# Performance work log

Measured on AMD Instinct MI355X. Metric: run time of the kernel, lower is better.

Reference implementation:

```python
import jax, jax.numpy as jnp
import numpy as np

B, CIN, H, W = 8, 128, 64, 64
COUT = 128
UP = 2
KH = KW = 2 * UP  # 4
K = KH * KW       # 16
HO, WO = H - KH + 1, W - KW + 1  # stride=1, padding=0 (defaults actually used)


def setup_inputs() -> dict:
    key = jax.random.key(0)
    k1, k2, k3, k4, k5 = jax.random.split(key, 5)
    inp = jax.random.normal(k1, (B, CIN, H, W), jnp.float32)
    offset = jax.random.normal(k2, (B, 2 * K, HO, WO), jnp.float32)
    mask = jax.random.uniform(k3, (B, K, HO, WO), jnp.float32)
    fan_in = CIN * KH * KW
    bound = 1.0 / np.sqrt(fan_in)  # kaiming_uniform(a=sqrt(5)) bound
    weight = jax.random.uniform(k4, (COUT, CIN, KH, KW), jnp.float32, -bound, bound)
    bias = jax.random.uniform(k5, (COUT,), jnp.float32, -bound, bound)
    return {"input": inp, "offset": offset, "mask": mask, "weight": weight, "bias": bias}


def _deform_conv(inp, offset, mask, weight, bias):
    # modulated deformable conv, groups=1, stride=1, pad=0, dilation=1
    b, cin, h, w = inp.shape
    ho, wo = offset.shape[2], offset.shape[3]
    k = mask.shape[1]
    off = offset.reshape(b, k, 2, ho, wo)
    dy, dx = off[:, :, 0], off[:, :, 1]              # [b,k,ho,wo]

    ki, kj = jnp.meshgrid(jnp.arange(KH), jnp.arange(KW), indexing="ij")
    ki = ki.reshape(k).astype(inp.dtype)
    kj = kj.reshape(k).astype(inp.dtype)

    # sampling coords: base output pixel + kernel tap + learned offset
    y = dy + ki[None, :, None, None] + jnp.arange(ho, dtype=inp.dtype)[None, None, :, None]
    x = dx + kj[None, :, None, None] + jnp.arange(wo, dtype=inp.dtype)[None, None, None, :]

    y0f = jnp.floor(y)
    x0f = jnp.floor(x)
    wy = y - y0f                                     # [b,k,ho,wo]
    wx = x - x0f
    y0 = y0f.astype(jnp.int32)
    x0 = x0f.astype(jnp.int32)

    inp_flat = inp.reshape(b, cin, h * w)

    def gather(yy, xx):
        valid = (yy >= 0) & (yy < h) & (xx >= 0) & (xx < w)
        idx = (jnp.clip(yy, 0, h - 1) * w + jnp.clip(xx, 0, w - 1)).reshape(b, -1)
        v = jnp.take_along_axis(inp_flat, idx[:, None, :], axis=2)
        v = v.reshape(b, cin, k, ho, wo)
        return v * valid[:, None].astype(inp.dtype)

    v00 = gather(y0, x0)
    v01 = gather(y0, x0 + 1)
    v10 = gather(y0 + 1, x0)
    v11 = gather(y0 + 1, x0 + 1)

    wy = wy[:, None]  # [b,1,k,ho,wo]
    wx = wx[:, None]
    sampled = (v00 * (1 - wy) * (1 - wx) + v01 * (1 - wy) * wx
               + v10 * wy * (1 - wx) + v11 * wy * wx)
    sampled = sampled * mask[:, None]                # mask modulation

    # weight is flipped in forward: weight.flip(-1, -2)
    w_flip = weight[:, :, ::-1, ::-1].reshape(weight.shape[0], cin, k)
    out = jnp.einsum("bckhw,ock->bohw", sampled, w_flip)
    return out + bias[None, :, None, None]


def reference(input, offset, mask, weight, bias):
    return _deform_conv(input, offset, mask, weight, bias)
```

## Files before the change

### kernel.cpp

```cpp
#include <hip/hip_runtime.h>
#include <hip/hip_bf16.h>

#define B_    8
#define CIN   128
#define H_    64
#define W_    64
#define COUT  128
#define K_    16
#define HO    61
#define WO    61
#define HW_   (HO * WO)

typedef short bf16x8 __attribute__((ext_vector_type(8)));
typedef short s16x4  __attribute__((ext_vector_type(4)));
typedef float f32x4  __attribute__((ext_vector_type(4)));
typedef float f32x4u __attribute__((ext_vector_type(4), aligned(4)));

#define B2F(s) __uint_as_float(((unsigned int)(unsigned short)(s)) << 16)

__global__ __launch_bounds__(256) void prep_all(const float* __restrict__ inp,
                                                const float* __restrict__ w,
                                                __hip_bfloat16* __restrict__ T,
                                                __hip_bfloat16* __restrict__ A2) {
    const int t = threadIdx.x;
    if (blockIdx.x < 512) {
        __shared__ float ld[64][129];
        const int b  = blockIdx.x >> 6;
        const int sb = (blockIdx.x & 63) << 6;
        const float* src = inp + ((size_t)b << 19);
        #pragma unroll
        for (int i = 0; i < 8; ++i) {
            int j  = i * 256 + t;
            int c  = j >> 4;
            int s4 = (j & 15) << 2;
            f32x4u v = *(const f32x4u*)(const void*)(src + ((size_t)c << 12) + sb + s4);
            #pragma unroll
            for (int q = 0; q < 4; ++q) ld[s4 + q][c] = v[q];
        }
        __syncthreads();
        __hip_bfloat16* dst = T + (((size_t)b << 12) + sb) * 128;
        #pragma unroll
        for (int i = 0; i < 8; ++i) {
            int j  = i * 256 + t;
            int s  = j >> 5;
            int c4 = (j & 31) << 2;
            s16x4 v;
            #pragma unroll
            for (int q = 0; q < 4; ++q) {
                __hip_bfloat16 hh = __float2bfloat16(ld[s][c4 + q]);
                v[q] = *reinterpret_cast<const short*>(&hh);
            }
            *(s16x4*)(void*)(dst + (size_t)s * 128 + c4) = v;
        }
    } else {
        int gid  = (blockIdx.x - 512) * 256 + t;
        int lane = gid & 63;
        int it   = (gid >> 6) & 63;
        int blk  = gid >> 12;
        int o    = blk * 16 + (lane & 15);
        int kk   = it * 32 + (lane >> 4) * 8;
        int k    = kk >> 7;
        int c0   = kk & 127;
        const float* srcw = w + (((size_t)(o << 7) + c0) << 4) + (15 - k);
        __hip_bfloat16* dst = A2 + (size_t)gid * 8;
        #pragma unroll
        for (int j = 0; j < 8; ++j)
            dst[j] = __float2bfloat16(srcw[j << 4]);
    }
}

__global__ __launch_bounds__(256, 3) void deform_gather(
        const __hip_bfloat16* __restrict__ T, const float* __restrict__ off,
        const float* __restrict__ msk, const __hip_bfloat16* __restrict__ A2,
        const float* __restrict__ bias, float* __restrict__ out) {

    __shared__ __align__(16) __hip_bfloat16 Bs[2][16 * 256];
    __shared__ float pw[4][256];
    __shared__ int   pb[2][256];

    const int t   = threadIdx.x;
    const int bid = blockIdx.x;
    const int b   = bid & 7;
    const int g   = bid >> 3;
    const int ho  = g >> 2;
    const int wt  = (g & 3) << 4;

    {
        const int p  = t & 15;
        const int k  = t >> 4;
        const int wo = wt + p;
        const bool pvalid = (wo < WO);
        const int wo_c = pvalid ? wo : (WO - 1);
        const int r    = ho * WO + wo_c;
        const int ki = k >> 2, kj = k & 3;
        const size_t offb = (size_t)b * (2 * K_ * HW_);
        float dy = off[offb + (size_t)(2 * k)     * HW_ + r];
        float dx = off[offb + (size_t)(2 * k + 1) * HW_ + r];
        float mm = msk[(size_t)b * (K_ * HW_) + (size_t)k * HW_ + r];
        if (!pvalid) mm = 0.0f;

        float y   = dy + (float)(ki + ho);
        float x   = dx + (float)(kj + wo_c);
        float y0f = floorf(y), x0f = floorf(x);
        float wy  = y - y0f,   wx  = x - x0f;
        int y0 = (int)y0f, x0 = (int)x0f;
        int y1 = y0 + 1,   x1 = x0 + 1;

        float wy0v = (1.0f - wy) * ((y0 >= 0 && y0 < H_) ? mm : 0.0f);
        float wy1v = wy          * ((y1 >= 0 && y1 < H_) ? mm : 0.0f);
        int cy0 = min(max(y0, 0), H_ - 1), cy1 = min(max(y1, 0), H_ - 1);

        float wx0v = (1.0f - wx) * ((x0 >= 0 && x0 < W_) ? 1.0f : 0.0f);
        float wx1v = wx          * ((x1 >= 0 && x1 < W_) ? 1.0f : 0.0f);
        int xb = min(max(x0, 0), W_ - 2);
        int tsh = x0 - xb;
        float a0 = (tsh == 0) ? wx0v : ((tsh == -1) ? wx1v : 0.0f);
        float a1 = (tsh == 0) ? wx1v : ((tsh ==  1) ? wx0v : 0.0f);

        pw[0][t] = wy0v * a0;  pw[1][t] = wy0v * a1;
        pw[2][t] = wy1v * a0;  pw[3][t] = wy1v * a1;
        pb[0][t] = (cy0 * W_ + xb) << 7;
        pb[1][t] = (cy1 * W_ + xb) << 7;
    }
    __syncthreads();

    const int lane = t & 63;
    const int wv   = t >> 6;
    const int p_g  = lane >> 2;
    const int cg_l = (lane & 3) << 3;
    const int mrow = lane & 15;
    const int quad = lane >> 4;
    const __hip_bfloat16* Tb = T + ((size_t)b << 19);
    const int u0 = wv, u1 = wv + 4;
    const int blk0 = 2 * wv, blk1 = 2 * wv + 1;

    f32x4 acc0 = {0.f, 0.f, 0.f, 0.f};
    f32x4 acc1 = {0.f, 0.f, 0.f, 0.f};

    auto uget = [&](int u, int h, bf16x8* cv, float* wts, int& swz) {
        const int tap  = 2 * h + (u >> 2);
        const int pair = (tap << 4) + p_g;
        wts[0] = pw[0][pair]; wts[1] = pw[1][pair];
        wts[2] = pw[2][pair]; wts[3] = pw[3][pair];
        const int cb = ((u & 3) << 5) + cg_l;
        const __hip_bfloat16* p0 = Tb + pb[0][pair] + cb;
        const __hip_bfloat16* p1 = Tb + pb[1][pair] + cb;
        cv[0] = *(const bf16x8*)(const void*)(p0);
        cv[1] = *(const bf16x8*)(const void*)(p0 + 128);
        cv[2] = *(const bf16x8*)(const void*)(p1);
        cv[3] = *(const bf16x8*)(const void*)(p1 + 128);
        const int kkl = ((u >> 2) << 7) + cb;
        swz = (p_g << 8) + ((kkl + (p_g << 3)) & 255);
    };

    auto ucombine = [&](const bf16x8* cv, const float* wts, int swz, int hb) {
        bf16x8 bb;
        #pragma unroll
        for (int q = 0; q < 8; ++q) {
            float s = wts[0] * B2F(cv[0][q]) + wts[1] * B2F(cv[1][q])
                    + wts[2] * B2F(cv[2][q]) + wts[3] * B2F(cv[3][q]);
            __hip_bfloat16 hh = __float2bfloat16(s);
            bb[q] = *reinterpret_cast<const short*>(&hh);
        }
        *(bf16x8*)(void*)(&Bs[hb][swz]) = bb;
    };

    bf16x8 avR[16];
    auto loadA = [&](int hp) {
        const __hip_bfloat16* a0 = A2 + ((size_t)((blk0 * 64 + hp * 8) * 64 + lane) << 3);
        const __hip_bfloat16* a1 = A2 + ((size_t)((blk1 * 64 + hp * 8) * 64 + lane) << 3);
        #pragma unroll
        for (int s_ = 0; s_ < 8; ++s_) {
            avR[2 * s_]     = *(const bf16x8*)(const void*)(a0 + ((size_t)s_ << 9));
            avR[2 * s_ + 1] = *(const bf16x8*)(const void*)(a1 + ((size_t)s_ << 9));
        }
    };
    auto mfma_exec = [&](int hp) {
        const int hb = hp & 1;
        #pragma unroll
        for (int s_ = 0; s_ < 8; ++s_) {
            const int idx = (mrow << 8) +
                            (((s_ << 5) + (quad << 3) + (mrow << 3)) & 255);
            bf16x8 bb = *(const bf16x8*)(const void*)(&Bs[hb][idx]);
            acc0 = __builtin_amdgcn_mfma_f32_16x16x32_bf16(avR[2 * s_],     bb, acc0, 0, 0, 0);
            acc1 = __builtin_amdgcn_mfma_f32_16x16x32_bf16(avR[2 * s_ + 1], bb, acc1, 0, 0, 0);
        }
    };

    bf16x8 cU0[4], cU1[4];
    float  wt0[4], wt1[4];
    int    sw0, sw1;

    uget(u0, 0, cU0, wt0, sw0);
    uget(u1, 0, cU1, wt1, sw1);
    ucombine(cU0, wt0, sw0, 0);
    ucombine(cU1, wt1, sw1, 0);
    __syncthreads();

    #pragma unroll 1
    for (int h = 1; h < 8; ++h) {
        loadA(h - 1);
        uget(u0, h, cU0, wt0, sw0);
        uget(u1, h, cU1, wt1, sw1);
        __builtin_amdgcn_s_setprio(1);
        mfma_exec(h - 1);
        __builtin_amdgcn_s_setprio(0);
        ucombine(cU0, wt0, sw0, h & 1);
        ucombine(cU1, wt1, sw1, h & 1);
        __syncthreads();
    }
    loadA(7);
    mfma_exec(7);

    const int wo = wt + mrow;
    if (wo < WO) {
        const size_t outb = (size_t)b * (COUT * HW_) + (size_t)(ho * WO + wo);
        #pragma unroll
        for (int jj = 0; jj < 4; ++jj) {
            int o0 = blk0 * 16 + quad * 4 + jj;
            int o1 = blk1 * 16 + quad * 4 + jj;
            out[outb + (size_t)o0 * HW_] = acc0[jj] + bias[o0];
            out[outb + (size_t)o1 * HW_] = acc1[jj] + bias[o1];
        }
    }
}

extern "C" void kernel_launch(void* const* d_in, const int* in_sizes, int n_in,
                              void* d_out, int out_size, void* d_ws, size_t ws_size,
                              hipStream_t stream) {
    const float* inp  = (const float*)d_in[0];
    const float* off  = (const float*)d_in[1];
    const float* msk  = (const float*)d_in[2];
    const float* wgt  = (const float*)d_in[3];
    const float* bias = (const float*)d_in[4];
    float* out = (float*)d_out;

    __hip_bfloat16* A2 = (__hip_bfloat16*)d_ws;
    __hip_bfloat16* T  = (__hip_bfloat16*)((char*)d_ws + (1 << 20));

    prep_all<<<640, 256, 0, stream>>>(inp, wgt, T, A2);

    int nblk = B_ * HO * 4;
    deform_gather<<<nblk, 256, 0, stream>>>(T, off, msk, A2, bias, out);
}
```

Baseline: 134.0 us.

## Double pixel tile per block to 32 to reuse weight fragments across MFMAs

Each block now covers 32 output pixels instead of 16, so every wave issues four MFMAs per loaded weight fragment and B tile. The count of weight (A2) loads per output is halved and the grid shrinks by half. The weight prefetch for the next step is also moved after the MFMA phase. In exchange the block needs twice the LDS and more registers per thread (16 gathered vectors plus 4 accumulators), which can lower occupancy, and fewer blocks run in total.

```diff
diff --git a/kernel.cpp b/kernel.cpp
--- a/kernel.cpp
+++ b/kernel.cpp
@@ -74,21 +74,23 @@
         const float* __restrict__ msk, const __hip_bfloat16* __restrict__ A2,
         const float* __restrict__ bias, float* __restrict__ out) {
 
-    __shared__ __align__(16) __hip_bfloat16 Bs[2][16 * 256];
-    __shared__ float pw[4][256];
-    __shared__ int   pb[2][256];
+    __shared__ __align__(16) __hip_bfloat16 Bs[2][32 * 256];
+    __shared__ float pw[4][512];
+    __shared__ int   pb[2][512];
 
     const int t   = threadIdx.x;
     const int bid = blockIdx.x;
     const int b   = bid & 7;
     const int g   = bid >> 3;
-    const int ho  = g >> 2;
-    const int wt  = (g & 3) << 4;
-
-    {
-        const int p  = t & 15;
-        const int k  = t >> 4;
-        const int wo = wt + p;
+    const int ho  = g >> 1;
+    const int wt  = (g & 1) << 5;
+
+    #pragma unroll
+    for (int ii = 0; ii < 2; ++ii) {
+        const int idx = ii * 256 + t;
+        const int px  = idx & 31;
+        const int k   = idx >> 5;
+        const int wo  = wt + px;
         const bool pvalid = (wo < WO);
         const int wo_c = pvalid ? wo : (WO - 1);
         const int r    = ho * WO + wo_c;
@@ -117,10 +119,10 @@
         float a0 = (tsh == 0) ? wx0v : ((tsh == -1) ? wx1v : 0.0f);
         float a1 = (tsh == 0) ? wx1v : ((tsh ==  1) ? wx0v : 0.0f);
 
-        pw[0][t] = wy0v * a0;  pw[1][t] = wy0v * a1;
-        pw[2][t] = wy1v * a0;  pw[3][t] = wy1v * a1;
-        pb[0][t] = (cy0 * W_ + xb) << 7;
-        pb[1][t] = (cy1 * W_ + xb) << 7;
+        pw[0][idx] = wy0v * a0;  pw[1][idx] = wy0v * a1;
+        pw[2][idx] = wy1v * a0;  pw[3][idx] = wy1v * a1;
+        pb[0][idx] = (cy0 * W_ + xb) << 7;
+        pb[1][idx] = (cy1 * W_ + xb) << 7;
     }
     __syncthreads();
 
@@ -131,38 +133,56 @@
     const int mrow = lane & 15;
     const int quad = lane >> 4;
     const __hip_bfloat16* Tb = T + ((size_t)b << 19);
-    const int u0 = wv, u1 = wv + 4;
     const int blk0 = 2 * wv, blk1 = 2 * wv + 1;
 
-    f32x4 acc0 = {0.f, 0.f, 0.f, 0.f};
-    f32x4 acc1 = {0.f, 0.f, 0.f, 0.f};
-
-    auto uget = [&](int u, int h, bf16x8* cv, float* wts, int& swz) {
-        const int tap  = 2 * h + (u >> 2);
-        const int pair = (tap << 4) + p_g;
-        wts[0] = pw[0][pair]; wts[1] = pw[1][pair];
-        wts[2] = pw[2][pair]; wts[3] = pw[3][pair];
-        const int cb = ((u & 3) << 5) + cg_l;
-        const __hip_bfloat16* p0 = Tb + pb[0][pair] + cb;
-        const __hip_bfloat16* p1 = Tb + pb[1][pair] + cb;
-        cv[0] = *(const bf16x8*)(const void*)(p0);
-        cv[1] = *(const bf16x8*)(const void*)(p0 + 128);
-        cv[2] = *(const bf16x8*)(const void*)(p1);
-        cv[3] = *(const bf16x8*)(const void*)(p1 + 128);
-        const int kkl = ((u >> 2) << 7) + cb;
-        swz = (p_g << 8) + ((kkl + (p_g << 3)) & 255);
-    };
-
-    auto ucombine = [&](const bf16x8* cv, const float* wts, int swz, int hb) {
-        bf16x8 bb;
-        #pragma unroll
-        for (int q = 0; q < 8; ++q) {
-            float s = wts[0] * B2F(cv[0][q]) + wts[1] * B2F(cv[1][q])
-                    + wts[2] * B2F(cv[2][q]) + wts[3] * B2F(cv[3][q]);
-            __hip_bfloat16 hh = __float2bfloat16(s);
-            bb[q] = *reinterpret_cast<const short*>(&hh);
-        }
-        *(bf16x8*)(void*)(&Bs[hb][swz]) = bb;
+    int tpar[4], cbU[4], pgU[4];
+    #pragma unroll
+    for (int i = 0; i < 4; ++i) {
+        const int u = (wv << 2) + i;
+        tpar[i] = u >> 3;
+        cbU[i]  = ((((u >> 1) & 3)) << 5) + cg_l;
+        pgU[i]  = u & 1;
+    }
+
+    f32x4 acc00 = {0.f,0.f,0.f,0.f}, acc01 = {0.f,0.f,0.f,0.f};
+    f32x4 acc10 = {0.f,0.f,0.f,0.f}, acc11 = {0.f,0.f,0.f,0.f};
+
+    bf16x8 cU[4][4];
+    float  wtU[4][4];
+    int    swzU[4];
+
+    auto uget_all = [&](int h) {
+        #pragma unroll
+        for (int i = 0; i < 4; ++i) {
+            const int tap  = 2 * h + tpar[i];
+            const int pidx = (tap << 5) + (pgU[i] << 4) + p_g;
+            wtU[i][0] = pw[0][pidx]; wtU[i][1] = pw[1][pidx];
+            wtU[i][2] = pw[2][pidx]; wtU[i][3] = pw[3][pidx];
+            const __hip_bfloat16* p0 = Tb + pb[0][pidx] + cbU[i];
+            const __hip_bfloat16* p1 = Tb + pb[1][pidx] + cbU[i];
+            cU[i][0] = *(const bf16x8*)(const void*)(p0);
+            cU[i][1] = *(const bf16x8*)(const void*)(p0 + 128);
+            cU[i][2] = *(const bf16x8*)(const void*)(p1);
+            cU[i][3] = *(const bf16x8*)(const void*)(p1 + 128);
+            const int kkl = (tpar[i] << 7) + cbU[i];
+            const int row = (pgU[i] << 4) + p_g;
+            swzU[i] = (row << 8) + ((kkl + (row << 3)) & 255);
+        }
+    };
+
+    auto ucomb_all = [&](int hb) {
+        #pragma unroll
+        for (int i = 0; i < 4; ++i) {
+            bf16x8 bbv;
+            #pragma unroll
+            for (int q = 0; q < 8; ++q) {
+                float s = wtU[i][0] * B2F(cU[i][0][q]) + wtU[i][1] * B2F(cU[i][1][q])
+                        + wtU[i][2] * B2F(cU[i][2][q]) + wtU[i][3] * B2F(cU[i][3][q]);
+                __hip_bfloat16 hh = __float2bfloat16(s);
+                bbv[q] = *reinterpret_cast<const short*>(&hh);
+            }
+            *(bf16x8*)(void*)(&Bs[hb][swzU[i]]) = bbv;
+        }
     };
 
     bf16x8 avR[16];
@@ -175,52 +195,56 @@
             avR[2 * s_ + 1] = *(const bf16x8*)(const void*)(a1 + ((size_t)s_ << 9));
         }
     };
+
     auto mfma_exec = [&](int hp) {
         const int hb = hp & 1;
         #pragma unroll
         for (int s_ = 0; s_ < 8; ++s_) {
-            const int idx = (mrow << 8) +
-                            (((s_ << 5) + (quad << 3) + (mrow << 3)) & 255);
-            bf16x8 bb = *(const bf16x8*)(const void*)(&Bs[hb][idx]);
-            acc0 = __builtin_amdgcn_mfma_f32_16x16x32_bf16(avR[2 * s_],     bb, acc0, 0, 0, 0);
-            acc1 = __builtin_amdgcn_mfma_f32_16x16x32_bf16(avR[2 * s_ + 1], bb, acc1, 0, 0, 0);
-        }
-    };
-
-    bf16x8 cU0[4], cU1[4];
-    float  wt0[4], wt1[4];
-    int    sw0, sw1;
-
-    uget(u0, 0, cU0, wt0, sw0);
-    uget(u1, 0, cU1, wt1, sw1);
-    ucombine(cU0, wt0, sw0, 0);
-    ucombine(cU1, wt1, sw1, 0);
+            const int base = (s_ << 5) + (quad << 3);
+            const int r0 = mrow;
+            const int r1 = 16 + mrow;
+            const int i0 = (r0 << 8) + ((base + (r0 << 3)) & 255);
+            const int i1 = (r1 << 8) + ((base + (r1 << 3)) & 255);
+            bf16x8 bb0 = *(const bf16x8*)(const void*)(&Bs[hb][i0]);
+            bf16x8 bb1 = *(const bf16x8*)(const void*)(&Bs[hb][i1]);
+            acc00 = __builtin_amdgcn_mfma_f32_16x16x32_bf16(avR[2*s_],   bb0, acc00, 0, 0, 0);
+            acc01 = __builtin_amdgcn_mfma_f32_16x16x32_bf16(avR[2*s_],   bb1, acc01, 0, 0, 0);
+            acc10 = __builtin_amdgcn_mfma_f32_16x16x32_bf16(avR[2*s_+1], bb0, acc10, 0, 0, 0);
+            acc11 = __builtin_amdgcn_mfma_f32_16x16x32_bf16(avR[2*s_+1], bb1, acc11, 0, 0, 0);
+        }
+    };
+
+    uget_all(0);
+    ucomb_all(0);
+    loadA(0);
     __syncthreads();
 
     #pragma unroll 1
     for (int h = 1; h < 8; ++h) {
-        loadA(h - 1);
-        uget(u0, h, cU0, wt0, sw0);
-        uget(u1, h, cU1, wt1, sw1);
+        uget_all(h);
         __builtin_amdgcn_s_setprio(1);
         mfma_exec(h - 1);
         __builtin_amdgcn_s_setprio(0);
-        ucombine(cU0, wt0, sw0, h & 1);
-        ucombine(cU1, wt1, sw1, h & 1);
+        loadA(h);
+        ucomb_all(h & 1);
         __syncthreads();
     }
-    loadA(7);
     mfma_exec(7);
 
-    const int wo = wt + mrow;
-    if (wo < WO) {
-        const size_t outb = (size_t)b * (COUT * HW_) + (size_t)(ho * WO + wo);
-        #pragma unroll
-        for (int jj = 0; jj < 4; ++jj) {
-            int o0 = blk0 * 16 + quad * 4 + jj;
-            int o1 = blk1 * 16 + quad * 4 + jj;
-            out[outb + (size_t)o0 * HW_] = acc0[jj] + bias[o0];
-            out[outb + (size_t)o1 * HW_] = acc1[jj] + bias[o1];
+    #pragma unroll
+    for (int pg = 0; pg < 2; ++pg) {
+        const int wo = wt + (pg << 4) + mrow;
+        if (wo < WO) {
+            const size_t outb = (size_t)b * (COUT * HW_) + (size_t)(ho * WO + wo);
+            const f32x4 a0 = pg ? acc01 : acc00;
+            const f32x4 a1 = pg ? acc11 : acc10;
+            #pragma unroll
+            for (int jj = 0; jj < 4; ++jj) {
+                int o0 = blk0 * 16 + quad * 4 + jj;
+                int o1 = blk1 * 16 + quad * 4 + jj;
+                out[outb + (size_t)o0 * HW_] = a0[jj] + bias[o0];
+                out[outb + (size_t)o1 * HW_] = a1[jj] + bias[o1];
+            }
         }
     }
 }
@@ -240,6 +264,6 @@
 
     prep_all<<<640, 256, 0, stream>>>(inp, wgt, T, A2);
 
-    int nblk = B_ * HO * 4;
+    int nblk = B_ * HO * 2;
     deform_gather<<<nblk, 256, 0, stream>>>(T, off, msk, A2, bias, out);
 }
```

Measured after the change: 158.8 us. 1.18x slower.
